# Kernel optimization log

Measured on AMD Instinct MI355X. Metric: run time of the kernel, lower is better.

The kernel has to match this reference:

```python
import jax, jax.numpy as jnp
import numpy as np


def setup_inputs() -> dict:
    key = jax.random.key(0)
    k1, k2 = jax.random.split(key)
    B, N, M, D = 4, 8192, 8192, 3
    prediction = jax.random.normal(k1, (B, N, D), dtype=jnp.float32)
    ground_truth = jax.random.normal(k2, (B, M, D), dtype=jnp.float32)
    return {"prediction": prediction, "ground_truth": ground_truth}


def reference(prediction, ground_truth):
    # Pairwise Euclidean distances via the expansion trick (avoids the
    x2 = jnp.sum(prediction * prediction, axis=-1)          # [B, N]
    y2 = jnp.sum(ground_truth * ground_truth, axis=-1)      # [B, M]
    xy = jnp.einsum('bnd,bmd->bnm', prediction, ground_truth)  # [B, N, M]
    d = jnp.sqrt(jnp.maximum(x2[..., :, None] + y2[..., None, :] - 2.0 * xy, 0.0))
    # Directed Hausdorff distances, then symmetric max.
    d_xy = jnp.max(jnp.min(d, axis=-1), axis=-1)  # max_n min_m  -> [B]
    d_yx = jnp.max(jnp.min(d, axis=-2), axis=-1)  # max_m min_n  -> [B]
    return jnp.maximum(d_xy, d_yx)
```

## Files before the change

### kernel.cpp

```cpp
#include <hip/hip_runtime.h>
#include <math.h>

#define BATCH 4
#define NPTS 8192
#define TB 256
#define XSPAN 64
#define XBLKS (NPTS / XSPAN)
#define CH 512
#define NCH (NPTS / CH)
#define TPC (CH / 32)

typedef _Float16 f16x8 __attribute__((ext_vector_type(8)));
typedef float f32x16 __attribute__((ext_vector_type(16)));


__device__ __forceinline__ float tree17(f32x16 d, float r) {
    float v0 = fminf(fminf(d[0], d[1]), d[2]);
    float v1 = fminf(fminf(d[3], d[4]), d[5]);
    float v2 = fminf(fminf(d[6], d[7]), d[8]);
    float v3 = fminf(fminf(d[9], d[10]), d[11]);
    float v4 = fminf(fminf(d[12], d[13]), d[14]);
    float w0 = fminf(fminf(v0, v1), v2);
    float w1 = fminf(fminf(v3, v4), d[15]);
    return fminf(fminf(w0, w1), r);
}

#define MFMA2(D0, D1, AF, BFa, BFb)                                           \
    asm volatile(                                                             \
        "s_nop 1\n\t"                                                         \
        "v_mfma_f32_32x32x16_f16 %0, %2, %3, %5\n\t"                          \
        "v_mfma_f32_32x32x16_f16 %1, %2, %4, %5\n\t"                          \
        "s_nop 7\n\t"                                                         \
        "s_nop 7\n\t"                                                         \
        "s_nop 1\n\t"                                                         \
        : "=&v"(D0), "=&v"(D1)                                                \
        : "v"(AF), "v"(BFa), "v"(BFb), "v"(zc));

__global__ __launch_bounds__(TB) void hd_one(const float* __restrict__ pred,
                                             const float* __restrict__ gt,
                                             unsigned* __restrict__ outbits) {
    const int tid = threadIdx.x;
    const int xblk = blockIdx.x;
    const int b = blockIdx.y;
    const int dir = blockIdx.z;

    const float* X = (dir == 0) ? pred + (size_t)b * NPTS * 3 : gt + (size_t)b * NPTS * 3;
    const float* Y = (dir == 0) ? gt + (size_t)b * NPTS * 3 : pred + (size_t)b * NPTS * 3;

    __shared__ __align__(16) _Float16 As[CH * 16];
    __shared__ float pmin[4][XSPAN];

    const int wave = tid >> 6, lane = tid & 63, half = lane >> 5, ln = lane & 31;
    const int xw = xblk * XSPAN;
    f16x8 bf0, bf1;
#pragma unroll
    for (int i = 0; i < 2; ++i) {
        int px = xw + i * 32 + ln;
        float x0 = X[3 * px], x1 = X[3 * px + 1], x2 = X[3 * px + 2];
        _Float16 h0 = (_Float16)x0, h1 = (_Float16)x1, h2 = (_Float16)x2;
        _Float16 l0 = (_Float16)(x0 - (float)h0);
        _Float16 l1 = (_Float16)(x1 - (float)h1);
        _Float16 l2 = (_Float16)(x2 - (float)h2);
        float xs = fmaf(x0, x0, fmaf(x1, x1, x2 * x2));
        _Float16 sh = (_Float16)xs, sl = (_Float16)(xs - (float)sh);
        f16x8 g0 = {h0, h1, h2, l0, l1, l2, h0, h1};
        f16x8 g1 = {h2, l0, l1, l2, (_Float16)1.f, (_Float16)1.f, sh, sl};
        if (i == 0) bf0 = half ? g1 : g0;
        else        bf1 = half ? g1 : g0;
    }

    const f32x16 zc = {0.f, 0.f, 0.f, 0.f, 0.f, 0.f, 0.f, 0.f,
                       0.f, 0.f, 0.f, 0.f, 0.f, 0.f, 0.f, 0.f};
    float rmin0 = 3.0e38f, rmin1 = 3.0e38f;

    for (int c = 0; c < NCH; ++c) {
        const int ybase = c * CH;
        for (int p = tid; p < CH; p += TB) {
            int gp = ybase + p;
            float y0 = Y[3 * gp], y1 = Y[3 * gp + 1], y2 = Y[3 * gp + 2];
            _Float16 h0 = (_Float16)y0, h1 = (_Float16)y1, h2 = (_Float16)y2;
            _Float16 l0 = (_Float16)(y0 - (float)h0);
            _Float16 l1 = (_Float16)(y1 - (float)h1);
            _Float16 l2 = (_Float16)(y2 - (float)h2);
            float ys = fmaf(y0, y0, fmaf(y1, y1, y2 * y2));
            _Float16 sh = (_Float16)ys, sl = (_Float16)(ys - (float)sh);
            const _Float16 n2 = (_Float16)(-2.f);
            _Float16 A0 = n2 * h0, A1 = n2 * h1, A2 = n2 * h2;
            _Float16 C0 = n2 * l0, C1 = n2 * l1, C2 = n2 * l2;
            f16x8 g0 = {A0, A1, A2, A0, A1, A2, C0, C1};
            f16x8 g1 = {C2, C0, C1, C2, sh, sl, (_Float16)1.f, (_Float16)1.f};
            int t = p >> 5, q = p & 31;
            *(f16x8*)&As[t * 512 + q * 8] = g0;
            *(f16x8*)&As[t * 512 + 256 + q * 8] = g1;
        }
        __syncthreads();

#pragma unroll
        for (int j = 0; j < 4; ++j) {
            int t = wave * 4 + j;
            f16x8 af = *(const f16x8*)&As[t * 512 + half * 256 + ln * 8];
            f32x16 d0, d1;
            MFMA2(d0, d1, af, bf0, bf1)
            rmin0 = tree17(d0, rmin0);
            rmin1 = tree17(d1, rmin1);
        }
        __syncthreads();
    }

    {
        float v0 = fminf(rmin0, __shfl_xor(rmin0, 32, 64));
        float v1 = fminf(rmin1, __shfl_xor(rmin1, 32, 64));
        if (lane < 32) {
            pmin[wave][ln] = v0;
            pmin[wave][32 + ln] = v1;
        }
    }
    __syncthreads();
    if (tid < 64) {
        float m = fminf(fminf(pmin[0][tid], pmin[1][tid]),
                        fminf(pmin[2][tid], pmin[3][tid]));
        m = fmaxf(m, 0.f);
#pragma unroll
        for (int off = 32; off > 0; off >>= 1)
            m = fmaxf(m, __shfl_xor(m, off, 64));
        if (tid == 0) atomicMax(&outbits[b], __float_as_uint(sqrtf(m)));
    }
}

extern "C" void kernel_launch(void* const* d_in, const int* in_sizes, int n_in,
                              void* d_out, int out_size, void* d_ws, size_t ws_size,
                              hipStream_t stream) {
    const float* pred = (const float*)d_in[0];
    const float* gt = (const float*)d_in[1];

    (void)hipMemsetAsync(d_out, 0, (size_t)out_size * sizeof(float), stream);
    hd_one<<<dim3(XBLKS, BATCH, 2), TB, 0, stream>>>(pred, gt, (unsigned*)d_out);
}
```

Measured before the change: 86.17 us.

## Double-buffer Y staging in LDS with register prefetch of next chunk

Splits the shared staging buffer into two halves and loads the next chunk's Y points into registers before running the MFMA work on the current chunk, then converts and stores them into the other buffer. This removes one of the two barriers per chunk and hides global load latency behind the matrix and min-reduction work. It doubles LDS use for the staging buffer and adds register pressure, which could lower occupancy.

```diff
diff --git a/kernel.cpp b/kernel.cpp
--- a/kernel.cpp
+++ b/kernel.cpp
@@ -8,7 +8,6 @@
 #define XBLKS (NPTS / XSPAN)
 #define CH 512
 #define NCH (NPTS / CH)
-#define TPC (CH / 32)
 
 typedef _Float16 f16x8 __attribute__((ext_vector_type(8)));
 typedef float f32x16 __attribute__((ext_vector_type(16)));
@@ -47,10 +46,28 @@
     const float* X = (dir == 0) ? pred + (size_t)b * NPTS * 3 : gt + (size_t)b * NPTS * 3;
     const float* Y = (dir == 0) ? gt + (size_t)b * NPTS * 3 : pred + (size_t)b * NPTS * 3;
 
-    __shared__ __align__(16) _Float16 As[CH * 16];
+    __shared__ __align__(16) _Float16 As[2][CH * 16];
     __shared__ float pmin[4][XSPAN];
 
     const int wave = tid >> 6, lane = tid & 63, half = lane >> 5, ln = lane & 31;
+
+    auto stage = [&](int buf, int p, float y0, float y1, float y2) {
+        _Float16 h0 = (_Float16)y0, h1 = (_Float16)y1, h2 = (_Float16)y2;
+        _Float16 l0 = (_Float16)(y0 - (float)h0);
+        _Float16 l1 = (_Float16)(y1 - (float)h1);
+        _Float16 l2 = (_Float16)(y2 - (float)h2);
+        float ys = fmaf(y0, y0, fmaf(y1, y1, y2 * y2));
+        _Float16 sh = (_Float16)ys, sl = (_Float16)(ys - (float)sh);
+        const _Float16 n2 = (_Float16)(-2.f);
+        _Float16 A0 = n2 * h0, A1 = n2 * h1, A2 = n2 * h2;
+        _Float16 C0 = n2 * l0, C1 = n2 * l1, C2 = n2 * l2;
+        f16x8 g0 = {A0, A1, A2, A0, A1, A2, C0, C1};
+        f16x8 g1 = {C2, C0, C1, C2, sh, sl, (_Float16)1.f, (_Float16)1.f};
+        int t = p >> 5, q = p & 31;
+        *(f16x8*)&As[buf][t * 512 + q * 8] = g0;
+        *(f16x8*)&As[buf][t * 512 + 256 + q * 8] = g1;
+    };
+
     const int xw = xblk * XSPAN;
     f16x8 bf0, bf1;
 #pragma unroll
@@ -69,40 +86,41 @@
         else        bf1 = half ? g1 : g0;
     }
 
+    {
+        float y0 = Y[3 * tid], y1 = Y[3 * tid + 1], y2 = Y[3 * tid + 2];
+        int p2 = tid + 256;
+        float z0 = Y[3 * p2], z1 = Y[3 * p2 + 1], z2 = Y[3 * p2 + 2];
+        stage(0, tid, y0, y1, y2);
+        stage(0, p2, z0, z1, z2);
+    }
+    __syncthreads();
+
     const f32x16 zc = {0.f, 0.f, 0.f, 0.f, 0.f, 0.f, 0.f, 0.f,
                        0.f, 0.f, 0.f, 0.f, 0.f, 0.f, 0.f, 0.f};
     float rmin0 = 3.0e38f, rmin1 = 3.0e38f;
 
     for (int c = 0; c < NCH; ++c) {
-        const int ybase = c * CH;
-        for (int p = tid; p < CH; p += TB) {
-            int gp = ybase + p;
-            float y0 = Y[3 * gp], y1 = Y[3 * gp + 1], y2 = Y[3 * gp + 2];
-            _Float16 h0 = (_Float16)y0, h1 = (_Float16)y1, h2 = (_Float16)y2;
-            _Float16 l0 = (_Float16)(y0 - (float)h0);
-            _Float16 l1 = (_Float16)(y1 - (float)h1);
-            _Float16 l2 = (_Float16)(y2 - (float)h2);
-            float ys = fmaf(y0, y0, fmaf(y1, y1, y2 * y2));
-            _Float16 sh = (_Float16)ys, sl = (_Float16)(ys - (float)sh);
-            const _Float16 n2 = (_Float16)(-2.f);
-            _Float16 A0 = n2 * h0, A1 = n2 * h1, A2 = n2 * h2;
-            _Float16 C0 = n2 * l0, C1 = n2 * l1, C2 = n2 * l2;
-            f16x8 g0 = {A0, A1, A2, A0, A1, A2, C0, C1};
-            f16x8 g1 = {C2, C0, C1, C2, sh, sl, (_Float16)1.f, (_Float16)1.f};
-            int t = p >> 5, q = p & 31;
-            *(f16x8*)&As[t * 512 + q * 8] = g0;
-            *(f16x8*)&As[t * 512 + 256 + q * 8] = g1;
+        const int cur = c & 1, nxt = cur ^ 1;
+        float y0, y1, y2, z0, z1, z2;
+        const bool more = (c + 1 < NCH);
+        if (more) {
+            int gp = (c + 1) * CH + tid;
+            y0 = Y[3 * gp]; y1 = Y[3 * gp + 1]; y2 = Y[3 * gp + 2];
+            int gq = gp + 256;
+            z0 = Y[3 * gq]; z1 = Y[3 * gq + 1]; z2 = Y[3 * gq + 2];
         }
-        __syncthreads();
-
 #pragma unroll
         for (int j = 0; j < 4; ++j) {
             int t = wave * 4 + j;
-            f16x8 af = *(const f16x8*)&As[t * 512 + half * 256 + ln * 8];
+            f16x8 af = *(const f16x8*)&As[cur][t * 512 + half * 256 + ln * 8];
             f32x16 d0, d1;
             MFMA2(d0, d1, af, bf0, bf1)
             rmin0 = tree17(d0, rmin0);
             rmin1 = tree17(d1, rmin1);
+        }
+        if (more) {
+            stage(nxt, tid, y0, y1, y2);
+            stage(nxt, tid + 256, z0, z1, z2);
         }
         __syncthreads();
     }
```

New measurement: 81.98 us. 1.05x faster.
